# Kernel optimization log

Hardware: AMD Instinct MI355X
Metric: run time of the kernel (lower is better)

## Reference

```python
import jax, jax.numpy as jnp
import numpy as np

N, E = 50000, 800000
IN, P, H, D, OUT = 128, 32, 4, 64, 64
NEG_SLOPE = 0.2


def setup_inputs() -> dict:
    key = jax.random.key(0)
    ks = jax.random.split(key, 18)
    pm = lambda k, shape: jax.random.normal(k, shape, jnp.float32) * 0.05
    return {
        "fvs": jax.random.normal(ks[0], (N, IN), jnp.float32),
        "pos_enc": jax.random.normal(ks[1], (N, P), jnp.float32),
        "src": jax.random.randint(ks[2], (E,), 0, N, jnp.int32),
        "dst": jax.random.randint(ks[3], (E,), 0, N, jnp.int32),
        "W0": pm(ks[4], (IN + P, H * D)), "al0": pm(ks[5], (H, D)), "ar0": pm(ks[6], (H, D)), "rW0": pm(ks[7], (IN + P, H * D)),
        "W1": pm(ks[8], (H * D + P, H * D)), "al1": pm(ks[9], (H, D)), "ar1": pm(ks[10], (H, D)), "rW1": pm(ks[11], (H * D + P, H * D)),
        "W2": pm(ks[12], (H * D + P, H * OUT)), "al2": pm(ks[13], (H, OUT)), "ar2": pm(ks[14], (H, OUT)), "rW2": pm(ks[15], (H * D + P, H * OUT)),
        "num_nodes": N,
    }


def gat_conv(h, src, dst, W, al, ar, rW, num_nodes):
    # DGL-style GATConv: fc -> per-node attn logits -> edge leaky_relu -> dst-segment softmax -> weighted aggregate -> residual -> elu
    heads, dh = al.shape
    feat = (h @ W).reshape(-1, heads, dh)                    # [N,H,D]
    el = jnp.einsum('nhd,hd->nh', feat, al)                  # [N,H]
    er = jnp.einsum('nhd,hd->nh', feat, ar)
    e = jax.nn.leaky_relu(el[src] + er[dst], NEG_SLOPE)      # [E,H]
    emax = jax.lax.stop_gradient(jax.ops.segment_max(e, dst, num_segments=num_nodes))
    ee = jnp.exp(e - emax[dst])
    denom = jax.ops.segment_sum(ee, dst, num_segments=num_nodes)
    alpha = ee / denom[dst]                                  # [E,H]
    msg = feat[src] * alpha[..., None]                       # [E,H,D]
    rst = jax.ops.segment_sum(msg, dst, num_segments=num_nodes)  # [N,H,D]
    rst = rst + (h @ rW).reshape(-1, heads, dh)              # residual projection
    return jax.nn.elu(rst)


def reference(fvs, pos_enc, src, dst, W0, al0, ar0, rW0, W1, al1, ar1, rW1, W2, al2, ar2, rW2, num_nodes):
    h = jnp.concatenate([fvs, pos_enc], axis=1)
    h = gat_conv(h, src, dst, W0, al0, ar0, rW0, num_nodes).reshape(num_nodes, -1)
    h = jnp.concatenate([h, pos_enc], axis=1)
    h = gat_conv(h, src, dst, W1, al1, ar1, rW1, num_nodes).reshape(num_nodes, -1)
    h = jnp.concatenate([h, pos_enc], axis=1)
    h = gat_conv(h, src, dst, W2, al2, ar2, rW2, num_nodes).mean(axis=1)  # mean over heads -> [N,out_ch]
    return (h, pos_enc)
```

## Files before the change

### kernel.cpp

```cpp
#include <hip/hip_runtime.h>
#include <hip/hip_bf16.h>
#include <math.h>

#define NHEAD 4
#define DHEAD 64
#define HD 256
#define PDIM 32
#define LDH 288

typedef __attribute__((ext_vector_type(8))) short bf16x8;
typedef __attribute__((ext_vector_type(4))) float f32x4;
typedef __attribute__((ext_vector_type(2))) float f32x2;

static __device__ inline ushort f2bf(float f) {
  unsigned u = __float_as_uint(f);
  unsigned r = (u + 0x7fffu + ((u >> 16) & 1u)) >> 16;
  return (ushort)r;
}
static __device__ inline float bf2f(ushort s) {
  return __uint_as_float((unsigned)s << 16);
}

__global__ void k_count(const int* __restrict__ dst, int* __restrict__ counts, int E) {
  int i = blockIdx.x * blockDim.x + threadIdx.x;
  if (i < E) atomicAdd(&counts[dst[i]], 1);
}

__global__ void k_scan1(const int* __restrict__ counts, int* __restrict__ excl,
                        int* __restrict__ bsum, int Nn) {
  __shared__ int buf[256];
  int b = blockIdx.x, t = threadIdx.x;
  int i = b * 256 + t;
  int v = (i < Nn) ? counts[i] : 0;
  buf[t] = v;
  __syncthreads();
  for (int off = 1; off < 256; off <<= 1) {
    int x = (t >= off) ? buf[t - off] : 0;
    __syncthreads();
    buf[t] += x;
    __syncthreads();
  }
  if (i < Nn) excl[i] = buf[t] - v;
  if (t == 255) bsum[b] = buf[255];
}

__global__ void k_scan2(int* __restrict__ bsum, int nb) {
  __shared__ int buf[256];
  int t = threadIdx.x;
  int v = (t < nb) ? bsum[t] : 0;
  buf[t] = v;
  __syncthreads();
  for (int off = 1; off < 256; off <<= 1) {
    int x = (t >= off) ? buf[t - off] : 0;
    __syncthreads();
    buf[t] += x;
    __syncthreads();
  }
  if (t < nb) bsum[t] = buf[t] - v;
}

__global__ void k_scan3(const int* __restrict__ excl, const int* __restrict__ bsum,
                        int* __restrict__ row_start, int Nn, int E) {
  int i = blockIdx.x * 256 + threadIdx.x;
  if (i < Nn) row_start[i] = excl[i] + bsum[blockIdx.x];
  if (i == 0) row_start[Nn] = E;
}

__global__ void k_scatter(const int* __restrict__ src, const int* __restrict__ dst,
                          const int* __restrict__ row_start, int* __restrict__ cursor,
                          int* __restrict__ esrc, int E) {
  int i = blockIdx.x * blockDim.x + threadIdx.x;
  if (i < E) {
    int d = dst[i];
    int pos = row_start[d] + atomicAdd(&cursor[d], 1);
    esrc[pos] = src[i];
  }
}

__global__ void k_build_h0(const float* __restrict__ fvs, const float* __restrict__ pe,
                           ushort* __restrict__ hbuf, int Nn) {
  int i = blockIdx.x * blockDim.x + threadIdx.x;
  int total = Nn * 160;
  if (i >= total) return;
  int n = i / 160, j = i - n * 160;
  float v = (j < 128) ? fvs[n * 128 + j] : pe[n * PDIM + (j - 128)];
  hbuf[n * LDH + j] = f2bf(v);
}

__global__ void k_pack(const float* __restrict__ W, ushort* __restrict__ Bp, int K) {
  int i = blockIdx.x * 256 + threadIdx.x;
  int total = (K >> 5) * 16 * 64;
  if (i >= total) return;
  int lane = i & 63;
  int cb = (i >> 6) & 15;
  int kb = i >> 10;
  int col = cb * 16 + (lane & 15);
  int kbase = kb * 32 + (lane >> 4) * 8;
  ushort v[8];
#pragma unroll
  for (int j = 0; j < 8; ++j) v[j] = f2bf(W[(size_t)(kbase + j) * HD + col]);
  *(uint4*)&Bp[(size_t)i * 8] = *(uint4*)v;
}

__global__ __launch_bounds__(256) void k_gemm(const ushort* __restrict__ X, int K,
                                              const ushort* __restrict__ Wp,
                                              const ushort* __restrict__ rWp,
                                              const float* __restrict__ al,
                                              const float* __restrict__ ar,
                                              unsigned char* __restrict__ featf8,
                                              ushort* __restrict__ rrb,
                                              float* __restrict__ el,
                                              float* __restrict__ er,
                                              int Nn) {
  __shared__ float lds[4][16 * 68];
  int t = threadIdx.x;
  int w = t >> 6, lane = t & 63;
  int mode = blockIdx.y;
  const ushort* Bp = mode ? rWp : Wp;
  int row0 = blockIdx.x * 64;
  int col0 = w * 64;
  int lr = lane & 15, lk = lane >> 4;

  int arow[4];
#pragma unroll
  for (int m = 0; m < 4; ++m) {
    int r = row0 + m * 16 + lr;
    arow[m] = (r < Nn) ? r : (Nn - 1);
  }

  f32x4 acc[4][4] = {};
  int nkb = K >> 5;
  for (int kb = 0; kb < nkb; ++kb) {
    int k0 = kb * 32;
    bf16x8 a[4], b[4];
#pragma unroll
    for (int m = 0; m < 4; ++m)
      a[m] = *(const bf16x8*)&X[(size_t)arow[m] * LDH + k0 + lk * 8];
#pragma unroll
    for (int n = 0; n < 4; ++n)
      b[n] = *(const bf16x8*)&Bp[(((size_t)kb * 16 + (col0 >> 4) + n) * 64 + lane) * 8];
#pragma unroll
    for (int m = 0; m < 4; ++m)
#pragma unroll
      for (int n = 0; n < 4; ++n)
        acc[m][n] = __builtin_amdgcn_mfma_f32_16x16x32_bf16(a[m], b[n], acc[m][n], 0, 0, 0);
  }

  if (mode == 0) {
    float alv[4], arv[4];
#pragma unroll
    for (int n = 0; n < 4; ++n) {
      alv[n] = al[col0 + n * 16 + (lane & 15)];
      arv[n] = ar[col0 + n * 16 + (lane & 15)];
    }
#pragma unroll
    for (int m = 0; m < 4; ++m)
#pragma unroll
      for (int reg = 0; reg < 4; ++reg) {
        float e1 = 0.f, e2 = 0.f;
#pragma unroll
        for (int n = 0; n < 4; ++n) {
          e1 = fmaf(acc[m][n][reg], alv[n], e1);
          e2 = fmaf(acc[m][n][reg], arv[n], e2);
        }
#pragma unroll
        for (int msk = 1; msk < 16; msk <<= 1) {
          e1 += __shfl_xor(e1, msk);
          e2 += __shfl_xor(e2, msk);
        }
        int row = row0 + m * 16 + (lane >> 4) * 4 + reg;
        if ((lane & 15) == 0 && row < Nn) {
          el[row * NHEAD + w] = e1;
          er[row * NHEAD + w] = e2;
        }
      }
  }

  float* L = &lds[w][0];
  int r16 = lane >> 2, cbase = (lane & 3) * 16;
#pragma unroll
  for (int m = 0; m < 4; ++m) {
#pragma unroll
    for (int n = 0; n < 4; ++n)
#pragma unroll
      for (int reg = 0; reg < 4; ++reg)
        L[((lane >> 4) * 4 + reg) * 68 + n * 16 + (lane & 15)] = acc[m][n][reg];
    __syncthreads();
    int row = row0 + m * 16 + r16;
    if (row < Nn) {
      float c[16];
#pragma unroll
      for (int j = 0; j < 16; ++j) c[j] = L[r16 * 68 + cbase + j];
      if (mode == 0) {
        unsigned d[4];
#pragma unroll
        for (int q = 0; q < 4; ++q) {
          unsigned v = 0;
          v = __builtin_amdgcn_cvt_pk_fp8_f32(c[q * 4 + 0], c[q * 4 + 1], v, false);
          v = __builtin_amdgcn_cvt_pk_fp8_f32(c[q * 4 + 2], c[q * 4 + 3], v, true);
          d[q] = v;
        }
        *(uint4*)&featf8[(size_t)row * HD + col0 + cbase] = make_uint4(d[0], d[1], d[2], d[3]);
      } else {
        ushort tmp[16];
#pragma unroll
        for (int j = 0; j < 16; ++j) tmp[j] = f2bf(c[j]);
        *(uint4*)&rrb[(size_t)row * HD + col0 + cbase] = *(uint4*)&tmp[0];
        *(uint4*)&rrb[(size_t)row * HD + col0 + cbase + 8] = *(uint4*)&tmp[8];
      }
    }
    __syncthreads();
  }
}

__global__ __launch_bounds__(256) void k_agg(const int* __restrict__ esrc,
                                             const int* __restrict__ row_start,
                                             const float* __restrict__ el,
                                             const float* __restrict__ er,
                                             const unsigned char* __restrict__ featf8,
                                             const ushort* __restrict__ rrb,
                                             const float* __restrict__ pe,
                                             ushort* __restrict__ hnext,
                                             float* __restrict__ out,
                                             int last, int Nn) {
  int w = threadIdx.x >> 6;
  int lane = threadIdx.x & 63;
  int n = blockIdx.x * 4 + w;
  if (n >= Nn) return;
  int g = lane >> 4;
  int l = lane & 15;
  int h = l >> 2;
  int beg = row_start[n], end = row_start[n + 1];
  float ern = er[n * NHEAD + h];

  float acc[16] = {};
  float dn = 0.f;
  for (int p = beg + g; p < end; p += 4) {
    int s = esrc[p];
    float lg = el[s * NHEAD + h] + ern;
    lg = (lg > 0.f) ? lg : 0.2f * lg;
    float wgt = __expf(lg);
    dn += wgt;
    uint4 u = *(const uint4*)(featf8 + (size_t)s * HD + l * 16);
#define DEC8(uu, j0)                                                          \
    {                                                                         \
      f32x2 f0 = __builtin_amdgcn_cvt_pk_f32_fp8((int)(uu), false);           \
      f32x2 f1 = __builtin_amdgcn_cvt_pk_f32_fp8((int)(uu), true);            \
      acc[j0 + 0] = fmaf(wgt, f0[0], acc[j0 + 0]);                            \
      acc[j0 + 1] = fmaf(wgt, f0[1], acc[j0 + 1]);                            \
      acc[j0 + 2] = fmaf(wgt, f1[0], acc[j0 + 2]);                            \
      acc[j0 + 3] = fmaf(wgt, f1[1], acc[j0 + 3]);                            \
    }
    DEC8(u.x, 0) DEC8(u.y, 4) DEC8(u.z, 8) DEC8(u.w, 12)
#undef DEC8
  }
  dn += __shfl_xor(dn, 16);
  dn += __shfl_xor(dn, 32);
#pragma unroll
  for (int j = 0; j < 16; ++j) {
    acc[j] += __shfl_xor(acc[j], 16);
    acc[j] += __shfl_xor(acc[j], 32);
  }

  bool has = (end > beg);
  ushort rv[16];
  *(uint4*)&rv[0] = *(const uint4*)&rrb[(size_t)n * HD + l * 16];
  *(uint4*)&rv[8] = *(const uint4*)&rrb[(size_t)n * HD + l * 16 + 8];
  float vres[16];
  float inv = has ? 1.f / dn : 0.f;
#pragma unroll
  for (int j = 0; j < 16; ++j) {
    float v = acc[j] * inv + bf2f(rv[j]);
    vres[j] = (v > 0.f) ? v : (__expf(v) - 1.f);
  }

  if (!last) {
    if (g == 0) {
      ushort o[16];
#pragma unroll
      for (int j = 0; j < 16; ++j) o[j] = f2bf(vres[j]);
      *(uint4*)&hnext[(size_t)n * LDH + l * 16] = *(uint4*)&o[0];
      *(uint4*)&hnext[(size_t)n * LDH + l * 16 + 8] = *(uint4*)&o[8];
      if (l < 2) {
        ushort o2[16];
#pragma unroll
        for (int j = 0; j < 16; ++j) o2[j] = f2bf(pe[n * PDIM + l * 16 + j]);
        *(uint4*)&hnext[(size_t)n * LDH + HD + l * 16] = *(uint4*)&o2[0];
        *(uint4*)&hnext[(size_t)n * LDH + HD + l * 16 + 8] = *(uint4*)&o2[8];
      }
    }
  } else {
#pragma unroll
    for (int j = 0; j < 16; ++j) {
      vres[j] += __shfl_xor(vres[j], 4);
      vres[j] += __shfl_xor(vres[j], 8);
      vres[j] *= 0.25f;
    }
    if (g == 0 && l < 4) {
#pragma unroll
      for (int q = 0; q < 4; ++q)
        *(float4*)&out[(size_t)n * DHEAD + l * 16 + q * 4] =
            make_float4(vres[q * 4], vres[q * 4 + 1], vres[q * 4 + 2], vres[q * 4 + 3]);
    }
    if (g == 0 && l >= 4 && l < 6) {
      int c0 = (l - 4) * 16;
#pragma unroll
      for (int q = 0; q < 4; ++q) {
        const float* ps = &pe[n * PDIM + c0 + q * 4];
        *(float4*)&out[(size_t)Nn * DHEAD + (size_t)n * PDIM + c0 + q * 4] =
            make_float4(ps[0], ps[1], ps[2], ps[3]);
      }
    }
  }
}

extern "C" void kernel_launch(void* const* d_in, const int* in_sizes, int n_in,
                              void* d_out, int out_size, void* d_ws, size_t ws_size,
                              hipStream_t stream) {
  const float* fvs = (const float*)d_in[0];
  const float* pe  = (const float*)d_in[1];
  const int* src = (const int*)d_in[2];
  const int* dst = (const int*)d_in[3];
  const float* W[3]  = {(const float*)d_in[4], (const float*)d_in[8],  (const float*)d_in[12]};
  const float* al[3] = {(const float*)d_in[5], (const float*)d_in[9],  (const float*)d_in[13]};
  const float* ar[3] = {(const float*)d_in[6], (const float*)d_in[10], (const float*)d_in[14]};
  const float* rW[3] = {(const float*)d_in[7], (const float*)d_in[11], (const float*)d_in[15]};
  int Nn = in_sizes[0] / 128;
  int E  = in_sizes[2];
  int Ks[3] = {160, 288, 288};
  int nb = (Nn + 255) / 256;

  char* ws = (char*)d_ws;
  size_t off = 0;
  auto alloc = [&](size_t bytes) {
    void* p = ws + off;
    off += (bytes + 255) & ~(size_t)255;
    return p;
  };
  ushort* hbuf  = (ushort*)alloc((size_t)Nn * LDH * 2);
  unsigned char* featf8 = (unsigned char*)alloc((size_t)Nn * HD);
  ushort* rrb = (ushort*)alloc((size_t)Nn * HD * 2);
  float* el   = (float*)alloc((size_t)Nn * NHEAD * 4);
  float* er   = (float*)alloc((size_t)Nn * NHEAD * 4);
  ushort* Wp  = (ushort*)alloc((size_t)9 * 16 * 64 * 8 * 2);
  ushort* rWp = (ushort*)alloc((size_t)9 * 16 * 64 * 8 * 2);
  int* counts    = (int*)alloc((size_t)Nn * 4);
  int* cursor    = (int*)alloc((size_t)Nn * 4);
  int* row_start = (int*)alloc((size_t)(Nn + 1) * 4);
  int* excl      = (int*)alloc((size_t)Nn * 4);
  int* bsum      = (int*)alloc((size_t)256 * 4);
  int* esrc      = (int*)alloc((size_t)E * 4);

  hipMemsetAsync(counts, 0, (size_t)Nn * 4, stream);
  hipMemsetAsync(cursor, 0, (size_t)Nn * 4, stream);
  k_count<<<(E + 255) / 256, 256, 0, stream>>>(dst, counts, E);
  k_scan1<<<nb, 256, 0, stream>>>(counts, excl, bsum, Nn);
  k_scan2<<<1, 256, 0, stream>>>(bsum, nb);
  k_scan3<<<nb, 256, 0, stream>>>(excl, bsum, row_start, Nn, E);
  k_scatter<<<(E + 255) / 256, 256, 0, stream>>>(src, dst, row_start, cursor, esrc, E);
  k_build_h0<<<(Nn * 160 + 255) / 256, 256, 0, stream>>>(fvs, pe, hbuf, Nn);

  float* out = (float*)d_out;
  for (int L = 0; L < 3; ++L) {
    int npack = (Ks[L] >> 5) * 16 * 64;
    k_pack<<<(npack + 255) / 256, 256, 0, stream>>>(W[L], Wp, Ks[L]);
    k_pack<<<(npack + 255) / 256, 256, 0, stream>>>(rW[L], rWp, Ks[L]);
    dim3 g((Nn + 63) / 64, 2);
    k_gemm<<<g, 256, 0, stream>>>(hbuf, Ks[L], Wp, rWp, al[L], ar[L],
                                  featf8, rrb, el, er, Nn);
    int last = (L == 2) ? 1 : 0;
    k_agg<<<(Nn + 3) / 4, 256, 0, stream>>>(esrc, row_start, el, er, featf8, rrb, pe,
                                            hbuf, out, last, Nn);
  }
}
```

Baseline: 367.8 us.

## Fold attention logits into GEMM, merge weight packing, unroll aggregation loop

Precomputes W·al and W·ar as an extra packed column block so attention logits come out of an MFMA instead of a shuffle reduction. Packs all six weight matrices in one launch up front, and runs both the feature and residual GEMMs in one 512-thread block instead of a 2D grid. The aggregation loop is unrolled two edges per iteration for more memory-level parallelism, and the input build is vectorised. Folding al/ar into bf16 weights changes logit rounding slightly.

```diff
diff --git a/kernel.cpp b/kernel.cpp
--- a/kernel.cpp
+++ b/kernel.cpp
@@ -7,6 +7,7 @@
 #define HD 256
 #define PDIM 32
 #define LDH 288
+#define NCB 17
 
 typedef __attribute__((ext_vector_type(8))) short bf16x8;
 typedef __attribute__((ext_vector_type(4))) float f32x4;
@@ -80,45 +81,74 @@
 __global__ void k_build_h0(const float* __restrict__ fvs, const float* __restrict__ pe,
                            ushort* __restrict__ hbuf, int Nn) {
   int i = blockIdx.x * blockDim.x + threadIdx.x;
-  int total = Nn * 160;
+  int total = Nn * 20;
   if (i >= total) return;
-  int n = i / 160, j = i - n * 160;
-  float v = (j < 128) ? fvs[n * 128 + j] : pe[n * PDIM + (j - 128)];
-  hbuf[n * LDH + j] = f2bf(v);
-}
-
-__global__ void k_pack(const float* __restrict__ W, ushort* __restrict__ Bp, int K) {
+  int n = i / 20, j8 = (i - n * 20) * 8;
+  const float* srcp = (j8 < 128) ? &fvs[n * 128 + j8] : &pe[n * PDIM + (j8 - 128)];
+  float4 a = *(const float4*)srcp;
+  float4 b = *(const float4*)(srcp + 4);
+  ushort o[8] = {f2bf(a.x), f2bf(a.y), f2bf(a.z), f2bf(a.w),
+                 f2bf(b.x), f2bf(b.y), f2bf(b.z), f2bf(b.w)};
+  *(uint4*)&hbuf[(size_t)n * LDH + j8] = *(uint4*)o;
+}
+
+struct PackArgs {
+  const float* W[6];
+  const float* al[6];
+  const float* ar[6];
+  int kboff[7];
+};
+
+__global__ void k_pack(PackArgs pa, ushort* __restrict__ Bp) {
   int i = blockIdx.x * 256 + threadIdx.x;
-  int total = (K >> 5) * 16 * 64;
+  int total = pa.kboff[6] * NCB * 64;
   if (i >= total) return;
   int lane = i & 63;
-  int cb = (i >> 6) & 15;
-  int kb = i >> 10;
-  int col = cb * 16 + (lane & 15);
+  int cb = (i >> 6) % NCB;
+  int kbg = i / (NCB * 64);
+  int m = 0;
+  while (kbg >= pa.kboff[m + 1]) ++m;
+  int kb = kbg - pa.kboff[m];
+  const float* W = pa.W[m];
   int kbase = kb * 32 + (lane >> 4) * 8;
   ushort v[8];
-#pragma unroll
-  for (int j = 0; j < 8; ++j) v[j] = f2bf(W[(size_t)(kbase + j) * HD + col]);
+  if (cb < 16) {
+    int col = cb * 16 + (lane & 15);
+#pragma unroll
+    for (int j = 0; j < 8; ++j) v[j] = f2bf(W[(size_t)(kbase + j) * HD + col]);
+  } else {
+    int c = lane & 15;
+    const float* a = (c < 4) ? pa.al[m] : ((c < 8) ? pa.ar[m] : nullptr);
+    int h = c & 3;
+#pragma unroll
+    for (int j = 0; j < 8; ++j) {
+      float s = 0.f;
+      if (a) {
+        const float* wr = &W[(size_t)(kbase + j) * HD + h * 64];
+        const float* av = &a[h * 64];
+        for (int d = 0; d < 64; ++d) s = fmaf(wr[d], av[d], s);
+      }
+      v[j] = f2bf(s);
+    }
+  }
   *(uint4*)&Bp[(size_t)i * 8] = *(uint4*)v;
 }
 
-__global__ __launch_bounds__(256) void k_gemm(const ushort* __restrict__ X, int K,
-                                              const ushort* __restrict__ Wp,
-                                              const ushort* __restrict__ rWp,
-                                              const float* __restrict__ al,
-                                              const float* __restrict__ ar,
+__global__ __launch_bounds__(512) void k_gemm(const ushort* __restrict__ X, int K,
+                                              const ushort* __restrict__ BpW,
+                                              const ushort* __restrict__ BprW,
                                               unsigned char* __restrict__ featf8,
                                               ushort* __restrict__ rrb,
                                               float* __restrict__ el,
                                               float* __restrict__ er,
                                               int Nn) {
-  __shared__ float lds[4][16 * 68];
+  __shared__ float lds[8][16 * 68];
   int t = threadIdx.x;
   int w = t >> 6, lane = t & 63;
-  int mode = blockIdx.y;
-  const ushort* Bp = mode ? rWp : Wp;
+  int mode = w >> 2;
+  const ushort* Bp = mode ? BprW : BpW;
   int row0 = blockIdx.x * 64;
-  int col0 = w * 64;
+  int col0 = (w & 3) * 64;
   int lr = lane & 15, lk = lane >> 4;
 
   int arow[4];
@@ -129,7 +159,9 @@
   }
 
   f32x4 acc[4][4] = {};
+  f32x4 acce[4] = {};
   int nkb = K >> 5;
+  int cb0 = col0 >> 4;
   for (int kb = 0; kb < nkb; ++kb) {
     int k0 = kb * 32;
     bf16x8 a[4], b[4];
@@ -138,40 +170,30 @@
       a[m] = *(const bf16x8*)&X[(size_t)arow[m] * LDH + k0 + lk * 8];
 #pragma unroll
     for (int n = 0; n < 4; ++n)
-      b[n] = *(const bf16x8*)&Bp[(((size_t)kb * 16 + (col0 >> 4) + n) * 64 + lane) * 8];
+      b[n] = *(const bf16x8*)&Bp[(((size_t)kb * NCB + cb0 + n) * 64 + lane) * 8];
 #pragma unroll
     for (int m = 0; m < 4; ++m)
 #pragma unroll
       for (int n = 0; n < 4; ++n)
         acc[m][n] = __builtin_amdgcn_mfma_f32_16x16x32_bf16(a[m], b[n], acc[m][n], 0, 0, 0);
-  }
-
-  if (mode == 0) {
-    float alv[4], arv[4];
-#pragma unroll
-    for (int n = 0; n < 4; ++n) {
-      alv[n] = al[col0 + n * 16 + (lane & 15)];
-      arv[n] = ar[col0 + n * 16 + (lane & 15)];
-    }
+    if (w == 0) {
+      bf16x8 be = *(const bf16x8*)&Bp[(((size_t)kb * NCB + 16) * 64 + lane) * 8];
+#pragma unroll
+      for (int m = 0; m < 4; ++m)
+        acce[m] = __builtin_amdgcn_mfma_f32_16x16x32_bf16(a[m], be, acce[m], 0, 0, 0);
+    }
+  }
+
+  if (w == 0) {
+    int c = lane & 15;
 #pragma unroll
     for (int m = 0; m < 4; ++m)
 #pragma unroll
       for (int reg = 0; reg < 4; ++reg) {
-        float e1 = 0.f, e2 = 0.f;
-#pragma unroll
-        for (int n = 0; n < 4; ++n) {
-          e1 = fmaf(acc[m][n][reg], alv[n], e1);
-          e2 = fmaf(acc[m][n][reg], arv[n], e2);
-        }
-#pragma unroll
-        for (int msk = 1; msk < 16; msk <<= 1) {
-          e1 += __shfl_xor(e1, msk);
-          e2 += __shfl_xor(e2, msk);
-        }
         int row = row0 + m * 16 + (lane >> 4) * 4 + reg;
-        if ((lane & 15) == 0 && row < Nn) {
-          el[row * NHEAD + w] = e1;
-          er[row * NHEAD + w] = e2;
+        if (row < Nn) {
+          if (c < 4) el[row * NHEAD + c] = acce[m][reg];
+          else if (c < 8) er[row * NHEAD + (c - 4)] = acce[m][reg];
         }
       }
   }
@@ -235,14 +257,7 @@
 
   float acc[16] = {};
   float dn = 0.f;
-  for (int p = beg + g; p < end; p += 4) {
-    int s = esrc[p];
-    float lg = el[s * NHEAD + h] + ern;
-    lg = (lg > 0.f) ? lg : 0.2f * lg;
-    float wgt = __expf(lg);
-    dn += wgt;
-    uint4 u = *(const uint4*)(featf8 + (size_t)s * HD + l * 16);
-#define DEC8(uu, j0)                                                          \
+#define DEC8(uu, j0, wgt)                                                     \
     {                                                                         \
       f32x2 f0 = __builtin_amdgcn_cvt_pk_f32_fp8((int)(uu), false);           \
       f32x2 f1 = __builtin_amdgcn_cvt_pk_f32_fp8((int)(uu), true);            \
@@ -251,9 +266,30 @@
       acc[j0 + 2] = fmaf(wgt, f1[0], acc[j0 + 2]);                            \
       acc[j0 + 3] = fmaf(wgt, f1[1], acc[j0 + 3]);                            \
     }
-    DEC8(u.x, 0) DEC8(u.y, 4) DEC8(u.z, 8) DEC8(u.w, 12)
+  int p = beg + g;
+  for (; p + 4 < end; p += 8) {
+    int s0 = esrc[p], s1 = esrc[p + 4];
+    float lg0 = el[s0 * NHEAD + h] + ern;
+    float lg1 = el[s1 * NHEAD + h] + ern;
+    lg0 = (lg0 > 0.f) ? lg0 : 0.2f * lg0;
+    lg1 = (lg1 > 0.f) ? lg1 : 0.2f * lg1;
+    float w0 = __expf(lg0), w1 = __expf(lg1);
+    dn += w0 + w1;
+    uint4 u0 = *(const uint4*)(featf8 + (size_t)s0 * HD + l * 16);
+    uint4 u1 = *(const uint4*)(featf8 + (size_t)s1 * HD + l * 16);
+    DEC8(u0.x, 0, w0) DEC8(u0.y, 4, w0) DEC8(u0.z, 8, w0) DEC8(u0.w, 12, w0)
+    DEC8(u1.x, 0, w1) DEC8(u1.y, 4, w1) DEC8(u1.z, 8, w1) DEC8(u1.w, 12, w1)
+  }
+  if (p < end) {
+    int s0 = esrc[p];
+    float lg0 = el[s0 * NHEAD + h] + ern;
+    lg0 = (lg0 > 0.f) ? lg0 : 0.2f * lg0;
+    float w0 = __expf(lg0);
+    dn += w0;
+    uint4 u0 = *(const uint4*)(featf8 + (size_t)s0 * HD + l * 16);
+    DEC8(u0.x, 0, w0) DEC8(u0.y, 4, w0) DEC8(u0.z, 8, w0) DEC8(u0.w, 12, w0)
+  }
 #undef DEC8
-  }
   dn += __shfl_xor(dn, 16);
   dn += __shfl_xor(dn, 32);
 #pragma unroll
@@ -342,8 +378,14 @@
   ushort* rrb = (ushort*)alloc((size_t)Nn * HD * 2);
   float* el   = (float*)alloc((size_t)Nn * NHEAD * 4);
   float* er   = (float*)alloc((size_t)Nn * NHEAD * 4);
-  ushort* Wp  = (ushort*)alloc((size_t)9 * 16 * 64 * 8 * 2);
-  ushort* rWp = (ushort*)alloc((size_t)9 * 16 * 64 * 8 * 2);
+  PackArgs pa;
+  int kbs[6] = {5, 5, 9, 9, 9, 9};
+  pa.kboff[0] = 0;
+  for (int m = 0; m < 6; ++m) pa.kboff[m + 1] = pa.kboff[m] + kbs[m];
+  pa.W[0] = W[0]; pa.W[1] = rW[0]; pa.W[2] = W[1]; pa.W[3] = rW[1]; pa.W[4] = W[2]; pa.W[5] = rW[2];
+  pa.al[0] = al[0]; pa.al[1] = nullptr; pa.al[2] = al[1]; pa.al[3] = nullptr; pa.al[4] = al[2]; pa.al[5] = nullptr;
+  pa.ar[0] = ar[0]; pa.ar[1] = nullptr; pa.ar[2] = ar[1]; pa.ar[3] = nullptr; pa.ar[4] = ar[2]; pa.ar[5] = nullptr;
+  ushort* Bp = (ushort*)alloc((size_t)pa.kboff[6] * NCB * 64 * 8 * 2);
   int* counts    = (int*)alloc((size_t)Nn * 4);
   int* cursor    = (int*)alloc((size_t)Nn * 4);
   int* row_start = (int*)alloc((size_t)(Nn + 1) * 4);
@@ -358,16 +400,16 @@
   k_scan2<<<1, 256, 0, stream>>>(bsum, nb);
   k_scan3<<<nb, 256, 0, stream>>>(excl, bsum, row_start, Nn, E);
   k_scatter<<<(E + 255) / 256, 256, 0, stream>>>(src, dst, row_start, cursor, esrc, E);
-  k_build_h0<<<(Nn * 160 + 255) / 256, 256, 0, stream>>>(fvs, pe, hbuf, Nn);
+  k_build_h0<<<(Nn * 20 + 255) / 256, 256, 0, stream>>>(fvs, pe, hbuf, Nn);
+  int npack = pa.kboff[6] * NCB * 64;
+  k_pack<<<(npack + 255) / 256, 256, 0, stream>>>(pa, Bp);
 
   float* out = (float*)d_out;
   for (int L = 0; L < 3; ++L) {
-    int npack = (Ks[L] >> 5) * 16 * 64;
-    k_pack<<<(npack + 255) / 256, 256, 0, stream>>>(W[L], Wp, Ks[L]);
-    k_pack<<<(npack + 255) / 256, 256, 0, stream>>>(rW[L], rWp, Ks[L]);
-    dim3 g((Nn + 63) / 64, 2);
-    k_gemm<<<g, 256, 0, stream>>>(hbuf, Ks[L], Wp, rWp, al[L], ar[L],
-                                  featf8, rrb, el, er, Nn);
+    const ushort* BpW  = Bp + (size_t)pa.kboff[2 * L] * NCB * 64 * 8;
+    const ushort* BprW = Bp + (size_t)pa.kboff[2 * L + 1] * NCB * 64 * 8;
+    k_gemm<<<(Nn + 63) / 64, 512, 0, stream>>>(hbuf, Ks[L], BpW, BprW,
+                                               featf8, rrb, el, er, Nn);
     int last = (L == 2) ? 1 : 0;
     k_agg<<<(Nn + 3) / 4, 256, 0, stream>>>(esrc, row_start, el, er, featf8, rrb, pe,
                                             hbuf, out, last, Nn);
```

Result: slower. 406.9 us (+10.6%).
